# Kernel tuning notes

Hardware: AMD Instinct MI355X
Metric: run time of the kernel (lower is better)

## Reference

```python
import jax, jax.numpy as jnp
import numpy as np

HEAD_SIZE = 64

def setup_inputs() -> dict:
    key = jax.random.key(0)
    ks = jax.random.split(key, 6)
    B, T, D, H, HS = 4, 2048, 1024, 16, HEAD_SIZE
    s = 1.0 / np.sqrt(D)
    return {
        "x": jax.random.normal(ks[0], (B, T, D), jnp.float32),
        "Wq": jax.random.normal(ks[1], (H, D, HS), jnp.float32) * s,
        "Wk": jax.random.normal(ks[2], (H, D, HS), jnp.float32) * s,
        "Wv": jax.random.normal(ks[3], (H, D, HS), jnp.float32) * s,
        "Wp": jax.random.normal(ks[4], (D, D), jnp.float32) * s,
        "bp": jnp.zeros((D,), jnp.float32),
    }

def reference(x, Wq, Wk, Wv, Wp, bp):
    B, T, D = x.shape
    H, _, HS = Wq.shape
    # per-head projections (bias-free Linears), stacked over heads
    q = jnp.einsum('btd,hde->bhte', x, Wq)
    k = jnp.einsum('btd,hde->bhte', x, Wk)
    v = jnp.einsum('btd,hde->bhte', x, Wv)
    scores = jnp.einsum('bhqe,bhke->bhqk', q, k) / jnp.sqrt(jnp.float32(HS))
    causal = jnp.tril(jnp.ones((T, T), bool))  # mask[:T,:T]
    scores = jnp.where(causal, scores, -jnp.inf)
    w = jax.nn.softmax(scores, axis=-1)  # dropout p=0.0 -> identity
    out = jnp.einsum('bhqk,bhke->bhqe', w, v)
    # concat heads along last dim: [B,T,H*HS] == [B,T,D]
    out = out.transpose(0, 2, 1, 3).reshape(B, T, H * HS)
    return out @ Wp.T + bp  # note: Wp stored as [out,in] like nn.Linear
```

## Files before the change

kernel.cpp:

```cpp
#include <hip/hip_runtime.h>
#include <hip/hip_bf16.h>

typedef unsigned short u16;
typedef unsigned int u32;
typedef __attribute__((ext_vector_type(8))) short short8;
typedef __attribute__((ext_vector_type(4))) float f32x4;

#define B_ 4
#define T_ 2048
#define D_ 1024
#define H_ 16
#define HS_ 64
#define BT (B_*T_)

__device__ __forceinline__ float bf2f(u16 b){ union{u32 u; float f;} v; v.u=((u32)b)<<16; return v.f; }
__device__ __forceinline__ u16 f2bf(float f){
    __hip_bfloat16 h = __float2bfloat16(f);
    union{__hip_bfloat16 h; u16 u;} v; v.h = h; return v.u;
}
__device__ __forceinline__ void split2(float x, u16& h, u16& l){
    u16 hb = f2bf(x);
    float fh = bf2f(hb);
    h = hb; l = f2bf(x - fh);
}
union U4 { u16 s[4]; uint2 v; };
union S8 { u16 s[8]; short8 v; };

#define GLD16(g,l) __builtin_amdgcn_global_load_lds( \
    (__attribute__((address_space(1))) void*)(u16*)(g), \
    (__attribute__((address_space(3))) void*)(l), 16, 0, 0)

__device__ __forceinline__ int swz(int row, int col){
    return row*64 + (((col>>3) ^ (row&7))<<3) + (col&7);
}
#define FCHK(r) (((r)>>1)&3)

#define DPPMV(x, ctrl) __int_as_float(__builtin_amdgcn_update_dpp(0, __float_as_int(x), (ctrl), 0xF, 0xF, true))

__global__ __launch_bounds__(256) void pack_w(const float* __restrict__ Wq,
                                              const float* __restrict__ Wk,
                                              const float* __restrict__ Wv,
                                              u16* __restrict__ Wth,
                                              u16* __restrict__ Wtl)
{
    __shared__ float Tl[64*68];
    const int h = blockIdx.x, dt = blockIdx.y, z = blockIdx.z;
    const float* src = (z==0) ? Wq : ((z==1) ? Wk : Wv);
    const int t = threadIdx.x;
    const int d0 = dt*64;
    #pragma unroll
    for (int i=0;i<4;++i){
        int ci = t + 256*i;
        int dr = ci>>4, ec = ci&15;
        float4 v = *(const float4*)(src + ((size_t)h*D_ + d0+dr)*HS_ + ec*4);
        *(float4*)(Tl + dr*68 + ec*4) = v;
    }
    __syncthreads();
    #pragma unroll
    for (int i=0;i<4;++i){
        int ci = t + 256*i;
        int e = ci>>4, dc = ci&15;
        U4 hh, ll;
        #pragma unroll
        for (int j=0;j<4;++j){
            float f = Tl[(dc*4+j)*68 + e];
            split2(f, hh.s[j], ll.s[j]);
        }
        int n = z*D_ + h*HS_ + e;
        *(uint2*)(Wth + (size_t)n*D_ + d0 + dc*4) = hh.v;
        *(uint2*)(Wtl + (size_t)n*D_ + d0 + dc*4) = ll.v;
    }
}

__global__ __launch_bounds__(256) void gemm_qkv(const float* __restrict__ x,
                                                const u16* __restrict__ Wth,
                                                const u16* __restrict__ Wtl,
                                                float* __restrict__ qo,
                                                u16* __restrict__ kho, u16* __restrict__ klo,
                                                u16* __restrict__ vth, u16* __restrict__ vtl)
{
    __shared__ u16 Ash[128*32], Asl[128*32];
    __shared__ u16 Bsh[128*32], Bsl[128*32];
    const int n0 = blockIdx.x*128, m0 = blockIdx.y*128;
    const int t = threadIdx.x;
    const int w = t>>6, lane = t&63, quad = lane>>4, l16 = lane&15;
    const int wm = (w>>1)*64, wn = (w&1)*64;
    f32x4 acc[4][4];
    #pragma unroll
    for (int i=0;i<4;++i)
        #pragma unroll
        for (int j=0;j<4;++j) acc[i][j] = (f32x4){0.f,0.f,0.f,0.f};
    for (int kt=0; kt<32; ++kt){
        const int k0 = kt*32;
        #pragma unroll
        for (int i=0;i<2;++i){
            int ci = t + 256*i;
            int row = ci>>2, c = ci&3;
            int cs = c ^ FCHK(row);
            GLD16(Wth + (size_t)(n0+row)*D_ + k0 + cs*8, Bsh + ci*8);
            GLD16(Wtl + (size_t)(n0+row)*D_ + k0 + cs*8, Bsl + ci*8);
        }
        #pragma unroll
        for (int i=0;i<4;++i){
            int ci = t + 256*i;
            int row = ci>>3, c4 = ci&7;
            float4 av = *(const float4*)(x + (size_t)(m0+row)*D_ + k0 + c4*4);
            U4 hh, ll;
            split2(av.x, hh.s[0], ll.s[0]); split2(av.y, hh.s[1], ll.s[1]);
            split2(av.z, hh.s[2], ll.s[2]); split2(av.w, hh.s[3], ll.s[3]);
            int off = row*32 + ((((c4>>1) ^ FCHK(row))<<3) | ((c4&1)<<2));
            *(uint2*)(Ash + off) = hh.v;
            *(uint2*)(Asl + off) = ll.v;
        }
        __syncthreads();
        short8 afh[4], afl[4], bfh[4], bfl[4];
        #pragma unroll
        for (int mi=0;mi<4;++mi){
            const int rr = wm+mi*16+l16;
            const int off = rr*32 + ((quad ^ FCHK(rr))<<3);
            afh[mi] = *(const short8*)(Ash + off);
            afl[mi] = *(const short8*)(Asl + off);
        }
        #pragma unroll
        for (int ni=0;ni<4;++ni){
            const int rr = wn+ni*16+l16;
            const int off = rr*32 + ((quad ^ FCHK(rr))<<3);
            bfh[ni] = *(const short8*)(Bsh + off);
            bfl[ni] = *(const short8*)(Bsl + off);
        }
        #pragma unroll
        for (int mi=0;mi<4;++mi)
            #pragma unroll
            for (int ni=0;ni<4;++ni){
                acc[mi][ni] = __builtin_amdgcn_mfma_f32_16x16x32_bf16(afh[mi], bfh[ni], acc[mi][ni], 0,0,0);
                acc[mi][ni] = __builtin_amdgcn_mfma_f32_16x16x32_bf16(afh[mi], bfl[ni], acc[mi][ni], 0,0,0);
                acc[mi][ni] = __builtin_amdgcn_mfma_f32_16x16x32_bf16(afl[mi], bfh[ni], acc[mi][ni], 0,0,0);
            }
        __syncthreads();
    }
    const int z = n0 >> 10;
    if (z == 0){
        #pragma unroll
        for (int ni=0;ni<4;++ni){
            const int nloc = (n0 & 1023) + wn + ni*16 + l16;
            #pragma unroll
            for (int mi=0;mi<4;++mi){
                const int row = m0 + wm + mi*16 + quad*4;
                #pragma unroll
                for (int r=0;r<4;++r)
                    qo[(size_t)(row+r)*D_ + nloc] = acc[mi][ni][r];
            }
        }
    } else if (z == 1){
        #pragma unroll
        for (int ni=0;ni<4;++ni){
            const int nloc = (n0 & 1023) + wn + ni*16 + l16;
            #pragma unroll
            for (int mi=0;mi<4;++mi){
                const int row = m0 + wm + mi*16 + quad*4;
                #pragma unroll
                for (int r=0;r<4;++r){
                    u16 hh, ll; split2(acc[mi][ni][r], hh, ll);
                    kho[(size_t)(row+r)*D_ + nloc] = hh;
                    klo[(size_t)(row+r)*D_ + nloc] = ll;
                }
            }
        }
    } else {
        #pragma unroll
        for (int ni=0;ni<4;++ni){
            const int nloc = (n0 & 1023) + wn + ni*16 + l16;
            const int hloc = nloc>>6, e = nloc&63;
            #pragma unroll
            for (int mi=0;mi<4;++mi){
                const int rowb = m0 + wm + mi*16 + quad*4;
                const int bidx = rowb >> 11, tloc = rowb & 2047;
                U4 hh, ll;
                #pragma unroll
                for (int r=0;r<4;++r) split2(acc[mi][ni][r], hh.s[r], ll.s[r]);
                const size_t adr = ((size_t)((bidx*16 + hloc)*64 + e))*T_ + tloc;
                *(uint2*)(vth + adr) = hh.v;
                *(uint2*)(vtl + adr) = ll.v;
            }
        }
    }
}

__global__ __launch_bounds__(256, 2) void attn(const float* __restrict__ qf,
                                            const u16* __restrict__ kh, const u16* __restrict__ kl,
                                            const u16* __restrict__ vth, const u16* __restrict__ vtl,
                                            float* __restrict__ att)
{
    __shared__ u16 Ksh[64*64], Ksl[64*64];
    __shared__ u16 Vsh[64*64], Vsl[64*64];
    __shared__ u16 Pb[4*16*64];
    const int bx = blockIdx.x, by = blockIdx.y;
    const int bh = ((by & 7) << 3) | bx;
    const int px = by >> 3;
    const int b = bh >> 4, h = bh & 15;
    const int t = threadIdx.x;
    const int w = t>>6, lane = t&63, quad = lane>>4, l16 = lane&15;

    u16* Pm = Pb + w*1024;

    const int srow0 = t>>3,        sc0 = t&7;
    const int srow1 = (t+256)>>3,  sc1 = t&7;
    const int slo0 = swz(srow0, sc0*8);
    const int slo1 = swz(srow1, sc1*8);
    uint4 pkh0, pkh1, pkl0, pkl1, pvh0, pvh1, pvl0, pvl1;
    {
        const size_t gk0 = ((size_t)(b*T_ + srow0))*D_ + h*64 + sc0*8;
        const size_t gk1 = ((size_t)(b*T_ + srow1))*D_ + h*64 + sc1*8;
        pkh0 = *(const uint4*)(kh + gk0);  pkh1 = *(const uint4*)(kh + gk1);
        pkl0 = *(const uint4*)(kl + gk0);  pkl1 = *(const uint4*)(kl + gk1);
        const size_t gv0 = ((size_t)(bh*64 + srow0))*T_ + sc0*8;
        const size_t gv1 = ((size_t)(bh*64 + srow1))*T_ + sc1*8;
        pvh0 = *(const uint4*)(vth + gv0); pvh1 = *(const uint4*)(vth + gv1);
        pvl0 = *(const uint4*)(vtl + gv0); pvl1 = *(const uint4*)(vtl + gv1);
    }

    #pragma unroll 1
    for (int seg=0; seg<2; ++seg){
        const int qi = seg ? px : (31 - px);
        const int qrow = qi*64 + w*16;

        short8 qh_[2], ql_[2];
        {
            const float* qp = qf + ((size_t)(b*T_ + qrow + l16))*D_ + h*64;
            #pragma unroll
            for (int ks=0;ks<2;++ks){
                float4 a0 = *(const float4*)(qp + ks*32 + quad*8);
                float4 a1 = *(const float4*)(qp + ks*32 + quad*8 + 4);
                S8 hh, ll;
                split2(a0.x, hh.s[0], ll.s[0]); split2(a0.y, hh.s[1], ll.s[1]);
                split2(a0.z, hh.s[2], ll.s[2]); split2(a0.w, hh.s[3], ll.s[3]);
                split2(a1.x, hh.s[4], ll.s[4]); split2(a1.y, hh.s[5], ll.s[5]);
                split2(a1.z, hh.s[6], ll.s[6]); split2(a1.w, hh.s[7], ll.s[7]);
                qh_[ks] = hh.v; ql_[ks] = ll.v;
            }
        }
        f32x4 o[4];
        #pragma unroll
        for (int i=0;i<4;++i) o[i] = (f32x4){0.f,0.f,0.f,0.f};
        float m_i[4], l_i[4];
        #pragma unroll
        for (int r=0;r<4;++r){ m_i[r] = -INFINITY; l_i[r] = 0.f; }

        const int kvT = qi + 1;
        for (int kvt=0; kvt<kvT; ++kvt){
            __syncthreads();
            *(uint4*)(Ksh + slo0) = pkh0;  *(uint4*)(Ksh + slo1) = pkh1;
            *(uint4*)(Ksl + slo0) = pkl0;  *(uint4*)(Ksl + slo1) = pkl1;
            *(uint4*)(Vsh + slo0) = pvh0;  *(uint4*)(Vsh + slo1) = pvh1;
            *(uint4*)(Vsl + slo0) = pvl0;  *(uint4*)(Vsl + slo1) = pvl1;
            const int nk = (kvt+1 < kvT) ? (kvt+1) : ((seg==0) ? 0 : -1);
            if (nk >= 0){
                const size_t gk0 = ((size_t)(b*T_ + nk*64 + srow0))*D_ + h*64 + sc0*8;
                const size_t gk1 = ((size_t)(b*T_ + nk*64 + srow1))*D_ + h*64 + sc1*8;
                pkh0 = *(const uint4*)(kh + gk0);  pkh1 = *(const uint4*)(kh + gk1);
                pkl0 = *(const uint4*)(kl + gk0);  pkl1 = *(const uint4*)(kl + gk1);
                const size_t gv0 = ((size_t)(bh*64 + srow0))*T_ + nk*64 + sc0*8;
                const size_t gv1 = ((size_t)(bh*64 + srow1))*T_ + nk*64 + sc1*8;
                pvh0 = *(const uint4*)(vth + gv0); pvh1 = *(const uint4*)(vth + gv1);
                pvl0 = *(const uint4*)(vtl + gv0); pvl1 = *(const uint4*)(vtl + gv1);
            }
            __syncthreads();

            float s[4][4];
            __builtin_amdgcn_s_setprio(1);
            #pragma unroll
            for (int ni=0;ni<4;++ni){
                f32x4 sa = (f32x4){0.f,0.f,0.f,0.f};
                const int row = ni*16 + l16;
                #pragma unroll
                for (int ks=0;ks<2;++ks){
                    const int co = swz(row, ks*32 + quad*8);
                    short8 k8h = *(const short8*)(Ksh + co);
                    short8 k8l = *(const short8*)(Ksl + co);
                    sa = __builtin_amdgcn_mfma_f32_16x16x32_bf16(qh_[ks], k8h, sa, 0,0,0);
                    sa = __builtin_amdgcn_mfma_f32_16x16x32_bf16(qh_[ks], k8l, sa, 0,0,0);
                    sa = __builtin_amdgcn_mfma_f32_16x16x32_bf16(ql_[ks], k8h, sa, 0,0,0);
                }
                #pragma unroll
                for (int r=0;r<4;++r) s[ni][r] = sa[r]*0.125f;
            }
            __builtin_amdgcn_s_setprio(0);
            if (kvt*64 + 63 > qrow){
                #pragma unroll
                for (int ni=0;ni<4;++ni){
                    const int colabs = kvt*64 + ni*16 + l16;
                    #pragma unroll
                    for (int r=0;r<4;++r){
                        const int rowabs = qrow + quad*4 + r;
                        if (colabs > rowabs) s[ni][r] = -INFINITY;
                    }
                }
            }
            float alpha[4];
            #pragma unroll
            for (int r=0;r<4;++r){
                float rm = fmaxf(fmaxf(s[0][r],s[1][r]), fmaxf(s[2][r],s[3][r]));
                rm = fmaxf(rm, DPPMV(rm, 0xB1));
                rm = fmaxf(rm, DPPMV(rm, 0x4E));
                rm = fmaxf(rm, DPPMV(rm, 0x124));
                rm = fmaxf(rm, DPPMV(rm, 0x128));
                const float mnew = fmaxf(m_i[r], rm);
                alpha[r] = __expf(m_i[r] - mnew);
                m_i[r] = mnew;
                #pragma unroll
                for (int ni=0;ni<4;++ni) s[ni][r] = __expf(s[ni][r] - mnew);
                float rs = s[0][r]+s[1][r]+s[2][r]+s[3][r];
                rs += DPPMV(rs, 0xB1);
                rs += DPPMV(rs, 0x4E);
                rs += DPPMV(rs, 0x124);
                rs += DPPMV(rs, 0x128);
                l_i[r] = l_i[r]*alpha[r] + rs;
            }
            #pragma unroll
            for (int ni=0;ni<4;++ni)
                #pragma unroll
                for (int r=0;r<4;++r) o[ni][r] *= alpha[r];

            u16 ph[4][4], pl[4][4];
            #pragma unroll
            for (int ni=0;ni<4;++ni)
                #pragma unroll
                for (int r=0;r<4;++r)
                    split2(s[ni][r], ph[ni][r], pl[ni][r]);
            #pragma unroll
            for (int ni=0;ni<4;++ni)
                #pragma unroll
                for (int r=0;r<4;++r)
                    Pm[swz(quad*4+r, ni*16 + l16)] = ph[ni][r];
            __asm__ volatile("s_waitcnt lgkmcnt(0)" ::: "memory");
            short8 pah[2], pal[2];
            #pragma unroll
            for (int ks=0;ks<2;++ks)
                pah[ks] = *(const short8*)(Pm + swz(l16, ks*32 + quad*8));
            __asm__ volatile("" ::: "memory");
            #pragma unroll
            for (int ni=0;ni<4;++ni)
                #pragma unroll
                for (int r=0;r<4;++r)
                    Pm[swz(quad*4+r, ni*16 + l16)] = pl[ni][r];
            __asm__ volatile("s_waitcnt lgkmcnt(0)" ::: "memory");
            #pragma unroll
            for (int ks=0;ks<2;++ks)
                pal[ks] = *(const short8*)(Pm + swz(l16, ks*32 + quad*8));
            __asm__ volatile("" ::: "memory");

            __builtin_amdgcn_s_setprio(1);
            #pragma unroll
            for (int ni=0;ni<4;++ni){
                const int row = ni*16 + l16;
                #pragma unroll
                for (int ks=0;ks<2;++ks){
                    const int co = swz(row, ks*32 + quad*8);
                    short8 v8h = *(const short8*)(Vsh + co);
                    short8 v8l = *(const short8*)(Vsl + co);
                    o[ni] = __builtin_amdgcn_mfma_f32_16x16x32_bf16(pah[ks], v8h, o[ni], 0,0,0);
                    o[ni] = __builtin_amdgcn_mfma_f32_16x16x32_bf16(pah[ks], v8l, o[ni], 0,0,0);
                    o[ni] = __builtin_amdgcn_mfma_f32_16x16x32_bf16(pal[ks], v8h, o[ni], 0,0,0);
                }
            }
            __builtin_amdgcn_s_setprio(0);
        }
        const size_t ob = (size_t)(b*T_ + qrow);
        #pragma unroll
        for (int ni=0;ni<4;++ni){
            const int col = h*64 + ni*16 + l16;
            #pragma unroll
            for (int r=0;r<4;++r)
                att[(ob + quad*4 + r)*D_ + col] = o[ni][r] / l_i[r];
        }
    }
}

__global__ __launch_bounds__(256) void gemm_bt(const float* __restrict__ A,
                                               const float* __restrict__ Bt,
                                               float* __restrict__ C,
                                               const float* __restrict__ bias,
                                               int M, int N, int K)
{
    __shared__ u16 Ash[128*32], Asl[128*32];
    __shared__ u16 Bsh[128*32], Bsl[128*32];
    const int n0 = blockIdx.x*128, m0 = blockIdx.y*128;
    const int t = threadIdx.x;
    const int w = t>>6, lane = t&63, quad = lane>>4, l16 = lane&15;
    const int wm = (w>>1)*64, wn = (w&1)*64;
    f32x4 acc[4][4];
    #pragma unroll
    for (int i=0;i<4;++i)
        #pragma unroll
        for (int j=0;j<4;++j) acc[i][j] = (f32x4){0.f,0.f,0.f,0.f};
    const int kT = K >> 5;
    for (int kt=0; kt<kT; ++kt){
        const int k0 = kt*32;
        #pragma unroll
        for (int i=0;i<4;++i){
            int ci = t + 256*i;
            int row = ci>>3, c4 = ci&7;
            float4 av = *(const float4*)(A  + (size_t)(m0+row)*K + k0 + c4*4);
            float4 bv = *(const float4*)(Bt + (size_t)(n0+row)*K + k0 + c4*4);
            U4 ah, al, bh, bl;
            split2(av.x, ah.s[0], al.s[0]); split2(av.y, ah.s[1], al.s[1]);
            split2(av.z, ah.s[2], al.s[2]); split2(av.w, ah.s[3], al.s[3]);
            split2(bv.x, bh.s[0], bl.s[0]); split2(bv.y, bh.s[1], bl.s[1]);
            split2(bv.z, bh.s[2], bl.s[2]); split2(bv.w, bh.s[3], bl.s[3]);
            int off = row*32 + ((((c4>>1) ^ FCHK(row))<<3) | ((c4&1)<<2));
            *(uint2*)(Ash + off) = ah.v;
            *(uint2*)(Asl + off) = al.v;
            *(uint2*)(Bsh + off) = bh.v;
            *(uint2*)(Bsl + off) = bl.v;
        }
        __syncthreads();
        short8 afh[4], afl[4], bfh[4], bfl[4];
        #pragma unroll
        for (int mi=0;mi<4;++mi){
            const int rr = wm+mi*16+l16;
            const int off = rr*32 + ((quad ^ FCHK(rr))<<3);
            afh[mi] = *(const short8*)(Ash + off);
            afl[mi] = *(const short8*)(Asl + off);
        }
        #pragma unroll
        for (int ni=0;ni<4;++ni){
            const int rr = wn+ni*16+l16;
            const int off = rr*32 + ((quad ^ FCHK(rr))<<3);
            bfh[ni] = *(const short8*)(Bsh + off);
            bfl[ni] = *(const short8*)(Bsl + off);
        }
        #pragma unroll
        for (int mi=0;mi<4;++mi)
            #pragma unroll
            for (int ni=0;ni<4;++ni){
                acc[mi][ni] = __builtin_amdgcn_mfma_f32_16x16x32_bf16(afh[mi], bfh[ni], acc[mi][ni], 0,0,0);
                acc[mi][ni] = __builtin_amdgcn_mfma_f32_16x16x32_bf16(afh[mi], bfl[ni], acc[mi][ni], 0,0,0);
                acc[mi][ni] = __builtin_amdgcn_mfma_f32_16x16x32_bf16(afl[mi], bfh[ni], acc[mi][ni], 0,0,0);
            }
        __syncthreads();
    }
    #pragma unroll
    for (int ni=0;ni<4;++ni){
        const int col = n0 + wn + ni*16 + l16;
        const float bv = bias ? bias[col] : 0.f;
        #pragma unroll
        for (int mi=0;mi<4;++mi){
            const int row = m0 + wm + mi*16 + quad*4;
            #pragma unroll
            for (int r=0;r<4;++r)
                C[(size_t)(row+r)*N + col] = acc[mi][ni][r] + bv;
        }
    }
}

extern "C" void kernel_launch(void* const* d_in, const int* in_sizes, int n_in,
                              void* d_out, int out_size, void* d_ws, size_t ws_size,
                              hipStream_t stream)
{
    const float* x  = (const float*)d_in[0];
    const float* Wq = (const float*)d_in[1];
    const float* Wk = (const float*)d_in[2];
    const float* Wv = (const float*)d_in[3];
    const float* Wp = (const float*)d_in[4];
    const float* bp = (const float*)d_in[5];
    float* out = (float*)d_out;

    float* q   = (float*)d_ws;
    u16*  kh   = (u16*)(q + (size_t)BT*D_);
    u16*  kl   = kh + (size_t)BT*D_;
    u16*  vth  = kl + (size_t)BT*D_;
    u16*  vtl  = vth + (size_t)BT*D_;
    float* att = (float*)(vtl + (size_t)BT*D_);
    u16*  Wth  = (u16*)att;
    u16*  Wtl  = Wth + (size_t)3072*D_;

    pack_w  <<<dim3(16,16,3), 256, 0, stream>>>(Wq, Wk, Wv, Wth, Wtl);
    gemm_qkv<<<dim3(24, BT/128), 256, 0, stream>>>(x, Wth, Wtl, q, kh, kl, vth, vtl);
    attn    <<<dim3(8, 128), 256, 0, stream>>>(q, kh, kl, vth, vtl, att);
    gemm_bt <<<dim3(8, BT/128), 256, 0, stream>>>(att, Wp, out, bp, BT, D_, D_);
}
```

Before: 501.5 us.

## Transpose QK^T MFMA so softmax rows reduce in-lane with vectorized P stores

Swaps the MFMA operands for the score product so each lane holds a query row's scores across kv columns. The row max and sum become mostly in-thread reductions plus two cross-quad shuffles, replacing four DPP steps per row for each of four rows. P is now written to LDS as 8-byte vector stores instead of scalar 2-byte stores. Alpha and the final normalizer have to be shuffled back into the output accumulator layout, which adds shuffle traffic.

```diff
diff --git a/kernel.cpp b/kernel.cpp
--- a/kernel.cpp
+++ b/kernel.cpp
@@ -34,8 +34,6 @@
     return row*64 + (((col>>3) ^ (row&7))<<3) + (col&7);
 }
 #define FCHK(r) (((r)>>1)&3)
-
-#define DPPMV(x, ctrl) __int_as_float(__builtin_amdgcn_update_dpp(0, __float_as_int(x), (ctrl), 0xF, 0xF, true))
 
 __global__ __launch_bounds__(256) void pack_w(const float* __restrict__ Wq,
                                               const float* __restrict__ Wk,
@@ -223,6 +221,7 @@
     for (int seg=0; seg<2; ++seg){
         const int qi = seg ? px : (31 - px);
         const int qrow = qi*64 + w*16;
+        const int q_abs = qrow + l16;
 
         short8 qh_[2], ql_[2];
         {
@@ -242,9 +241,7 @@
         f32x4 o[4];
         #pragma unroll
         for (int i=0;i<4;++i) o[i] = (f32x4){0.f,0.f,0.f,0.f};
-        float m_i[4], l_i[4];
-        #pragma unroll
-        for (int r=0;r<4;++r){ m_i[r] = -INFINITY; l_i[r] = 0.f; }
+        float m_i = -INFINITY, l_i = 0.f;
 
         const int kvT = qi + 1;
         for (int kvt=0; kvt<kvT; ++kvt){
@@ -277,9 +274,9 @@
                     const int co = swz(row, ks*32 + quad*8);
                     short8 k8h = *(const short8*)(Ksh + co);
                     short8 k8l = *(const short8*)(Ksl + co);
-                    sa = __builtin_amdgcn_mfma_f32_16x16x32_bf16(qh_[ks], k8h, sa, 0,0,0);
-                    sa = __builtin_amdgcn_mfma_f32_16x16x32_bf16(qh_[ks], k8l, sa, 0,0,0);
-                    sa = __builtin_amdgcn_mfma_f32_16x16x32_bf16(ql_[ks], k8h, sa, 0,0,0);
+                    sa = __builtin_amdgcn_mfma_f32_16x16x32_bf16(k8h, qh_[ks], sa, 0,0,0);
+                    sa = __builtin_amdgcn_mfma_f32_16x16x32_bf16(k8l, qh_[ks], sa, 0,0,0);
+                    sa = __builtin_amdgcn_mfma_f32_16x16x32_bf16(k8h, ql_[ks], sa, 0,0,0);
                 }
                 #pragma unroll
                 for (int r=0;r<4;++r) s[ni][r] = sa[r]*0.125f;
@@ -288,50 +285,51 @@
             if (kvt*64 + 63 > qrow){
                 #pragma unroll
                 for (int ni=0;ni<4;++ni){
-                    const int colabs = kvt*64 + ni*16 + l16;
                     #pragma unroll
                     for (int r=0;r<4;++r){
-                        const int rowabs = qrow + quad*4 + r;
-                        if (colabs > rowabs) s[ni][r] = -INFINITY;
+                        const int kv_abs = kvt*64 + ni*16 + quad*4 + r;
+                        if (kv_abs > q_abs) s[ni][r] = -INFINITY;
                     }
                 }
             }
-            float alpha[4];
-            #pragma unroll
-            for (int r=0;r<4;++r){
-                float rm = fmaxf(fmaxf(s[0][r],s[1][r]), fmaxf(s[2][r],s[3][r]));
-                rm = fmaxf(rm, DPPMV(rm, 0xB1));
-                rm = fmaxf(rm, DPPMV(rm, 0x4E));
-                rm = fmaxf(rm, DPPMV(rm, 0x124));
-                rm = fmaxf(rm, DPPMV(rm, 0x128));
-                const float mnew = fmaxf(m_i[r], rm);
-                alpha[r] = __expf(m_i[r] - mnew);
-                m_i[r] = mnew;
-                #pragma unroll
-                for (int ni=0;ni<4;++ni) s[ni][r] = __expf(s[ni][r] - mnew);
-                float rs = s[0][r]+s[1][r]+s[2][r]+s[3][r];
-                rs += DPPMV(rs, 0xB1);
-                rs += DPPMV(rs, 0x4E);
-                rs += DPPMV(rs, 0x124);
-                rs += DPPMV(rs, 0x128);
-                l_i[r] = l_i[r]*alpha[r] + rs;
-            }
+            float rm = s[0][0];
             #pragma unroll
             for (int ni=0;ni<4;++ni)
                 #pragma unroll
-                for (int r=0;r<4;++r) o[ni][r] *= alpha[r];
-
-            u16 ph[4][4], pl[4][4];
+                for (int r=0;r<4;++r) rm = fmaxf(rm, s[ni][r]);
+            rm = fmaxf(rm, __shfl_xor(rm, 16));
+            rm = fmaxf(rm, __shfl_xor(rm, 32));
+            const float mnew = fmaxf(m_i, rm);
+            const float alpha = __expf(m_i - mnew);
+            m_i = mnew;
+            float rs = 0.f;
             #pragma unroll
             for (int ni=0;ni<4;++ni)
                 #pragma unroll
-                for (int r=0;r<4;++r)
-                    split2(s[ni][r], ph[ni][r], pl[ni][r]);
+                for (int r=0;r<4;++r){
+                    s[ni][r] = __expf(s[ni][r] - mnew);
+                    rs += s[ni][r];
+                }
+            rs += __shfl_xor(rs, 16);
+            rs += __shfl_xor(rs, 32);
+            l_i = l_i*alpha + rs;
+            float a4[4];
+            #pragma unroll
+            for (int r=0;r<4;++r) a4[r] = __shfl(alpha, quad*4 + r);
             #pragma unroll
             for (int ni=0;ni<4;++ni)
                 #pragma unroll
-                for (int r=0;r<4;++r)
-                    Pm[swz(quad*4+r, ni*16 + l16)] = ph[ni][r];
+                for (int r=0;r<4;++r) o[ni][r] *= a4[r];
+
+            uint2 plv[4];
+            #pragma unroll
+            for (int ni=0;ni<4;++ni){
+                U4 hh, ll;
+                #pragma unroll
+                for (int r=0;r<4;++r) split2(s[ni][r], hh.s[r], ll.s[r]);
+                *(uint2*)(Pm + swz(l16, ni*16 + quad*4)) = hh.v;
+                plv[ni] = ll.v;
+            }
             __asm__ volatile("s_waitcnt lgkmcnt(0)" ::: "memory");
             short8 pah[2], pal[2];
             #pragma unroll
@@ -340,9 +338,7 @@
             __asm__ volatile("" ::: "memory");
             #pragma unroll
             for (int ni=0;ni<4;++ni)
-                #pragma unroll
-                for (int r=0;r<4;++r)
-                    Pm[swz(quad*4+r, ni*16 + l16)] = pl[ni][r];
+                *(uint2*)(Pm + swz(l16, ni*16 + quad*4)) = plv[ni];
             __asm__ volatile("s_waitcnt lgkmcnt(0)" ::: "memory");
             #pragma unroll
             for (int ks=0;ks<2;++ks)
@@ -365,13 +361,16 @@
             }
             __builtin_amdgcn_s_setprio(0);
         }
+        float lt[4];
+        #pragma unroll
+        for (int r=0;r<4;++r) lt[r] = __shfl(l_i, quad*4 + r);
         const size_t ob = (size_t)(b*T_ + qrow);
         #pragma unroll
         for (int ni=0;ni<4;++ni){
             const int col = h*64 + ni*16 + l16;
             #pragma unroll
             for (int r=0;r<4;++r)
-                att[(ob + quad*4 + r)*D_ + col] = o[ni][r] / l_i[r];
+                att[(ob + quad*4 + r)*D_ + col] = o[ni][r] / lt[r];
         }
     }
 }
```

New measurement: 491.8 us. Within noise of the previous version (-1.9%).
